# Kernel tuning notes

Measured on AMD Instinct MI355X. Metric: run time of the kernel, lower is better.

The kernel has to match this reference:

```python
import jax, jax.numpy as jnp
import numpy as np

B = 1_000_000
H = 64
TARGET = 0.62562059 * 10.0  # self.target * scale
# GRN constants from NETC_high.__init__
A1, A2, B1C, B2C, K, NEXP, S, SCALE = 1.0, 1.0, 0.2, 0.2, 1.1, 2, 0.5, 10.0


def setup_inputs() -> dict:
    key = jax.random.key(0)
    ks = jax.random.split(key, 10)
    def xavier(k, shape):
        fan_in, fan_out = shape[1], shape[0]
        std = (2.0 / (fan_in + fan_out)) ** 0.5
        return std * jax.random.normal(k, shape, dtype=jnp.float32)
    return {
        "x": jax.random.uniform(ks[0], (B,), dtype=jnp.float32) * 10.0,
        "y": jax.random.uniform(ks[1], (B,), dtype=jnp.float32) * 10.0,
        "e_x": 0.1 * jax.random.normal(ks[2], (B,), dtype=jnp.float32),
        "e_y": 0.1 * jax.random.normal(ks[3], (B,), dtype=jnp.float32),
        "W1": xavier(ks[4], (H, 2)),
        "b1": jnp.zeros((H,), dtype=jnp.float32),
        "W2": xavier(ks[5], (H, H)),
        "b2": jnp.zeros((H,), dtype=jnp.float32),
        "W3": xavier(ks[6], (1, H)),
        "b3": jnp.zeros((1,), dtype=jnp.float32),
    }


def _mlp(z, W1, b1, W2, b2, W3, b3):
    # ControlNet.function: Linear->ReLU->Linear->ReLU->Linear
    h = jax.nn.relu(z @ W1.T + b1)
    h = jax.nn.relu(h @ W2.T + b2)
    return h @ W3.T + b3  # [*, 1]


def _control(inp, W1, b1, W2, b2, W3, b3):
    # ControlNet.forward: u(x) - u(target)
    tgt = jnp.full((1, 2), TARGET, dtype=inp.dtype)
    return _mlp(inp, W1, b1, W2, b2, W3, b3) - _mlp(tgt, W1, b1, W2, b2, W3, b3)


def reference(x, y, e_x, e_y, W1, b1, W2, b2, W3, b3):
    inp = jnp.stack([x + e_x, y + e_y], axis=-1)  # [B, 2]
    u = _control(inp, W1, b1, W2, b2, W3, b3)[:, 0]  # [B]
    xs = x / SCALE
    ys = y / SCALE
    s2 = S ** NEXP
    hx = xs ** NEXP / (s2 + xs ** NEXP)   # Hill activation in x
    hy = ys ** NEXP / (s2 + ys ** NEXP)
    gx = s2 / (s2 + xs ** NEXP)           # Hill repression by x
    gy = s2 / (s2 + ys ** NEXP)
    dx = SCALE * (A1 * hx + B1C * gy - K * xs + u * hx)
    dy = SCALE * (A2 * hy + B2C * gx - K * ys)
    return (dx, dy, -dx, -dy)
```

## Files before the change

kernel.cpp:

```cpp
#include <hip/hip_runtime.h>

#define BTOT 1000000

typedef _Float16 f16;
typedef f16 f16x2 __attribute__((ext_vector_type(2)));
typedef f16 f16x8 __attribute__((ext_vector_type(8)));
typedef float f32x2 __attribute__((ext_vector_type(2)));
typedef float f32x4 __attribute__((ext_vector_type(4)));

#define WS_BFRAG 16
#define WS_W1A   8208
#define WS_W1B   10256
#define WS_B1P   12304
#define WS_W3V   14352
#define WS_B2V   15376

template<int CTRL>
__device__ __forceinline__ float dpp_add(float v) {
    int pv = __builtin_amdgcn_update_dpp(0, __builtin_bit_cast(int, v),
                                         CTRL, 0xF, 0xF, true);
    return v + __builtin_bit_cast(float, pv);
}
__device__ __forceinline__ float row_reduce16(float p) {
    p = dpp_add<0x128>(p);
    p = dpp_add<0x124>(p);
    p = dpp_add<0x122>(p);
    p = dpp_add<0x121>(p);
    return p;
}

__global__ __launch_bounds__(256) void setup_kernel(
    const float* __restrict__ W1, const float* __restrict__ b1,
    const float* __restrict__ W2, const float* __restrict__ b2,
    const float* __restrict__ W3, unsigned char* __restrict__ ws)
{
    const int tid  = threadIdx.x;
    const int quad = (tid & 63) >> 4;
    const int nl   = tid & 15;

    __shared__ float w2s[64 * 65];
    __shared__ float h1s[64];
    __shared__ float part[4 * 64];

    const float4* W2v = (const float4*)W2;
    #pragma unroll
    for (int r = 0; r < 4; ++r) {
        int idx = r * 256 + tid;
        float4 f = W2v[idx];
        int g = idx * 4, row = g >> 6, col = g & 63;
        float* p = &w2s[row * 65 + col];
        p[0] = f.x; p[1] = f.y; p[2] = f.z; p[3] = f.w;
    }
    const float T = 6.2562059f;
    if (tid < 64)
        h1s[tid] = fmaxf(0.f, W1[2 * tid] * T + W1[2 * tid + 1] * T + b1[tid]);
    __syncthreads();

    {
        int r = tid & 63, kq = tid >> 6;
        float p = 0.f;
        #pragma unroll
        for (int k = 0; k < 16; ++k)
            p = fmaf(w2s[r * 65 + kq * 16 + k], h1s[kq * 16 + k], p);
        part[kq * 64 + r] = p;
    }
    __syncthreads();
    if (tid < 64) {
        float h2 = b2[tid] + part[tid] + part[64 + tid] + part[128 + tid] + part[192 + tid];
        float pr = fmaxf(0.f, h2) * W3[tid];
        #pragma unroll
        for (int m = 1; m < 64; m <<= 1) pr += __shfl_xor(pr, m, 64);
        if (tid == 0) *(float*)ws = pr;
    }

    if (tid < 64) {
        f16x8* bfragT = (f16x8*)(ws + WS_BFRAG);
        #pragma unroll
        for (int n = 0; n < 4; ++n)
            #pragma unroll
            for (int ks = 0; ks < 2; ++ks) {
                f16x8 f;
                #pragma unroll
                for (int j = 0; j < 8; ++j)
                    f[j] = (f16)w2s[(n * 16 + nl) * 65 + ks * 32 + quad * 8 + j];
                bfragT[(n * 2 + ks) * 64 + tid] = f;
            }
        f16x2* w1aT = (f16x2*)(ws + WS_W1A);
        f16x2* w1bT = (f16x2*)(ws + WS_W1B);
        f16x2* b1pT = (f16x2*)(ws + WS_B1P);
        #pragma unroll
        for (int i = 0; i < 8; ++i) {
            int kk = (i < 4) ? (quad * 8 + 2 * i) : (32 + quad * 8 + 2 * (i - 4));
            w1aT[i * 64 + tid] = f16x2{(f16)W1[2 * kk],     (f16)W1[2 * kk + 2]};
            w1bT[i * 64 + tid] = f16x2{(f16)W1[2 * kk + 1], (f16)W1[2 * kk + 3]};
            b1pT[i * 64 + tid] = f16x2{(f16)b1[kk],         (f16)b1[kk + 1]};
        }
        float* w3vT = (float*)(ws + WS_W3V);
        float* b2vT = (float*)(ws + WS_B2V);
        #pragma unroll
        for (int n = 0; n < 4; ++n) {
            w3vT[n * 64 + tid] = W3[n * 16 + nl];
            b2vT[n * 64 + tid] = b2[n * 16 + nl];
        }
    }
}

__global__ __launch_bounds__(256, 4) void netc_kernel(
    const float* __restrict__ x,  const float* __restrict__ y,
    const float* __restrict__ ex, const float* __restrict__ ey,
    const unsigned char* __restrict__ ws,
    float* __restrict__ out)
{
    const int tid  = threadIdx.x;
    const int lane = tid & 63;
    const int wv   = tid >> 6;
    const int quad = lane >> 4;
    const int nl   = lane & 15;

    const float u_tgt = *(const float*)ws;
    const float one_minus_ut = 1.0f - u_tgt;
    const f16x8* bfragT = (const f16x8*)(ws + WS_BFRAG);
    f16x8 bfrag[4][2];
    #pragma unroll
    for (int n = 0; n < 4; ++n)
        #pragma unroll
        for (int ks = 0; ks < 2; ++ks)
            bfrag[n][ks] = bfragT[(n * 2 + ks) * 64 + lane];
    const f16x2* w1aT = (const f16x2*)(ws + WS_W1A);
    const f16x2* w1bT = (const f16x2*)(ws + WS_W1B);
    const f16x2* b1pT = (const f16x2*)(ws + WS_B1P);
    f16x2 w1a[8], w1b[8], b1p[8];
    #pragma unroll
    for (int i = 0; i < 8; ++i) {
        w1a[i] = w1aT[i * 64 + lane];
        w1b[i] = w1bT[i * 64 + lane];
        b1p[i] = b1pT[i * 64 + lane];
    }
    const float* w3vT = (const float*)(ws + WS_W3V);
    const float* b2vT = (const float*)(ws + WS_B2V);
    float w3v[4], b2v[4];
    #pragma unroll
    for (int n = 0; n < 4; ++n) { w3v[n] = w3vT[n * 64 + lane]; b2v[n] = b2vT[n * 64 + lane]; }

    const f16x2 zero2 = {(f16)0.f, (f16)0.f};
    const int nwaves = (gridDim.x * blockDim.x) >> 6;
    const int estep  = nwaves << 6;
    const int srcb = (((nl >> 2) << 4) + quad * 4 + (nl & 3)) << 2;

    int e0 = (((blockIdx.x << 2) + wv) << 6) + lane;

    float axv = 0.f, ayv = 0.f, aexv = 0.f, aeyv = 0.f;
    float bxv = 0.f, byv = 0.f, bexv = 0.f, beyv = 0.f;
    if (e0 < BTOT)         { axv = x[e0]; ayv = y[e0]; aexv = ex[e0]; aeyv = ey[e0]; }
    if (e0 + estep < BTOT) { int p = e0 + estep; bxv = x[p]; byv = y[p]; bexv = ex[p]; beyv = ey[p]; }

    auto body = [&](int ee, float& rx, float& ry, float& rex, float& rey) {
        float cx = rx, cy = ry, cex = rex, cey = rey;
        int pe = ee + 2 * estep;
        if (pe < BTOT) { rx = x[pe]; ry = y[pe]; rex = ex[pe]; rey = ey[pe]; }

        float av = cx + cex, bv = cy + cey;
        f16x2 pab = {(f16)av, (f16)bv};
        int pv = __builtin_bit_cast(int, pab);

        float xs = cx * 0.1f, ys = cy * 0.1f;
        float x2 = xs * xs, y2 = ys * ys;
        float invx = __fdividef(1.0f, 0.25f + x2);
        float invy = __fdividef(1.0f, 0.25f + y2);
        float hx = x2 * invx, hy = y2 * invy;
        float gx = 0.25f * invx, gy = 0.25f * invy;
        float cdx = 10.f * hx;
        float base_dx = fmaf(cdx, one_minus_ut, fmaf(2.f, gy, -11.f * xs));
        float dy = fmaf(10.f, hy, fmaf(2.f, gx, -11.f * ys));
        out[BTOT + ee]     = dy;
        out[3 * BTOT + ee] = -dy;

        f16x2 pt[4];
        #pragma unroll
        for (int t = 0; t < 4; ++t)
            pt[t] = __builtin_bit_cast(f16x2,
                __builtin_amdgcn_ds_bpermute((t * 16 + nl) << 2, pv));

        float ur[4];
        #pragma unroll
        for (int t = 0; t < 4; ++t) {
            f32x4 acc[4];
            #pragma unroll
            for (int n = 0; n < 4; ++n)
                acc[n] = f32x4{b2v[n], b2v[n], b2v[n], b2v[n]};

            f16x2 a2 = {pt[t][0], pt[t][0]};
            f16x2 bb = {pt[t][1], pt[t][1]};
            union { f16x2 h2[8]; f16x8 fr[2]; } u;
            #pragma unroll
            for (int i = 0; i < 8; ++i) {
                f16x2 h = a2 * w1a[i] + (bb * w1b[i] + b1p[i]);
                u.h2[i] = __builtin_elementwise_max(h, zero2);
            }
            #pragma unroll
            for (int n = 0; n < 4; ++n) {
                acc[n] = __builtin_amdgcn_mfma_f32_16x16x32_f16(u.fr[0], bfrag[n][0], acc[n], 0, 0, 0);
                acc[n] = __builtin_amdgcn_mfma_f32_16x16x32_f16(u.fr[1], bfrag[n][1], acc[n], 0, 0, 0);
            }

            f32x2 p01 = {0.f, 0.f}, p23 = {0.f, 0.f};
            #pragma unroll
            for (int n = 0; n < 4; ++n) {
                f32x2 lo = {acc[n][0], acc[n][1]};
                f32x2 hi = {acc[n][2], acc[n][3]};
                lo = __builtin_elementwise_max(lo, f32x2{0.f, 0.f});
                hi = __builtin_elementwise_max(hi, f32x2{0.f, 0.f});
                f32x2 w = {w3v[n], w3v[n]};
                p01 += lo * w;
                p23 += hi * w;
            }
            float u0 = row_reduce16(p01[0]);
            float u1 = row_reduce16(p01[1]);
            float u2 = row_reduce16(p23[0]);
            float u3 = row_reduce16(p23[1]);
            float v01 = (nl & 1) ? u1 : u0;
            float v23 = (nl & 1) ? u3 : u2;
            ur[t] = (nl & 2) ? v23 : v01;
        }

        float s01  = (nl & 4) ? ur[1] : ur[0];
        float s23  = (nl & 4) ? ur[3] : ur[2];
        float send = (nl & 8) ? s23 : s01;
        float u_raw = __builtin_bit_cast(float,
            __builtin_amdgcn_ds_bpermute(srcb, __builtin_bit_cast(int, send)));

        float dx = fmaf(cdx, u_raw, base_dx);
        out[ee]            = dx;
        out[2 * BTOT + ee] = -dx;
    };

    for (int e = e0; e < BTOT; e += 2 * estep) {
        body(e, axv, ayv, aexv, aeyv);
        int e1 = e + estep;
        if (e1 < BTOT)
            body(e1, bxv, byv, bexv, beyv);
    }
}

extern "C" void kernel_launch(void* const* d_in, const int* in_sizes, int n_in,
                              void* d_out, int out_size, void* d_ws, size_t ws_size,
                              hipStream_t stream) {
    const float* x  = (const float*)d_in[0];
    const float* y  = (const float*)d_in[1];
    const float* ex = (const float*)d_in[2];
    const float* ey = (const float*)d_in[3];
    const float* W1 = (const float*)d_in[4];
    const float* b1 = (const float*)d_in[5];
    const float* W2 = (const float*)d_in[6];
    const float* b2 = (const float*)d_in[7];
    const float* W3 = (const float*)d_in[8];
    float* out = (float*)d_out;
    unsigned char* ws = (unsigned char*)d_ws;

    setup_kernel<<<1, 256, 0, stream>>>(W1, b1, W2, b2, W3, ws);
    netc_kernel<<<1024, 256, 0, stream>>>(x, y, ex, ey, ws, out);
}
```

Before: 105.1 us.

## Fuse weight setup into main kernel, use DPP transpose-reduce, raise MFMA priority

Drops the separate single-block setup kernel. Each block now computes u(target) and builds its own fp16 MFMA fragments from W1/W2 in shared memory, which removes a launch and the serial dependency on the workspace. The four 16-lane row reductions per tile are replaced by a butterfly exchange (swap-and-add across xor-1/xor-2 lanes, then row shifts), which cuts the number of DPP ops. It also brackets the MFMA sequence with s_setprio. The trade-off is that every block redundantly recomputes the target MLP and adds about 17KB of shared memory, which may limit occupancy.

```diff
diff --git a/kernel.cpp b/kernel.cpp
--- a/kernel.cpp
+++ b/kernel.cpp
@@ -8,107 +8,27 @@
 typedef float f32x2 __attribute__((ext_vector_type(2)));
 typedef float f32x4 __attribute__((ext_vector_type(4)));
 
-#define WS_BFRAG 16
-#define WS_W1A   8208
-#define WS_W1B   10256
-#define WS_B1P   12304
-#define WS_W3V   14352
-#define WS_B2V   15376
-
 template<int CTRL>
 __device__ __forceinline__ float dpp_add(float v) {
     int pv = __builtin_amdgcn_update_dpp(0, __builtin_bit_cast(int, v),
                                          CTRL, 0xF, 0xF, true);
     return v + __builtin_bit_cast(float, pv);
 }
-__device__ __forceinline__ float row_reduce16(float p) {
-    p = dpp_add<0x128>(p);
-    p = dpp_add<0x124>(p);
-    p = dpp_add<0x122>(p);
-    p = dpp_add<0x121>(p);
-    return p;
-}
-
-__global__ __launch_bounds__(256) void setup_kernel(
-    const float* __restrict__ W1, const float* __restrict__ b1,
-    const float* __restrict__ W2, const float* __restrict__ b2,
-    const float* __restrict__ W3, unsigned char* __restrict__ ws)
-{
-    const int tid  = threadIdx.x;
-    const int quad = (tid & 63) >> 4;
-    const int nl   = tid & 15;
-
-    __shared__ float w2s[64 * 65];
-    __shared__ float h1s[64];
-    __shared__ float part[4 * 64];
-
-    const float4* W2v = (const float4*)W2;
-    #pragma unroll
-    for (int r = 0; r < 4; ++r) {
-        int idx = r * 256 + tid;
-        float4 f = W2v[idx];
-        int g = idx * 4, row = g >> 6, col = g & 63;
-        float* p = &w2s[row * 65 + col];
-        p[0] = f.x; p[1] = f.y; p[2] = f.z; p[3] = f.w;
-    }
-    const float T = 6.2562059f;
-    if (tid < 64)
-        h1s[tid] = fmaxf(0.f, W1[2 * tid] * T + W1[2 * tid + 1] * T + b1[tid]);
-    __syncthreads();
-
-    {
-        int r = tid & 63, kq = tid >> 6;
-        float p = 0.f;
-        #pragma unroll
-        for (int k = 0; k < 16; ++k)
-            p = fmaf(w2s[r * 65 + kq * 16 + k], h1s[kq * 16 + k], p);
-        part[kq * 64 + r] = p;
-    }
-    __syncthreads();
-    if (tid < 64) {
-        float h2 = b2[tid] + part[tid] + part[64 + tid] + part[128 + tid] + part[192 + tid];
-        float pr = fmaxf(0.f, h2) * W3[tid];
-        #pragma unroll
-        for (int m = 1; m < 64; m <<= 1) pr += __shfl_xor(pr, m, 64);
-        if (tid == 0) *(float*)ws = pr;
-    }
-
-    if (tid < 64) {
-        f16x8* bfragT = (f16x8*)(ws + WS_BFRAG);
-        #pragma unroll
-        for (int n = 0; n < 4; ++n)
-            #pragma unroll
-            for (int ks = 0; ks < 2; ++ks) {
-                f16x8 f;
-                #pragma unroll
-                for (int j = 0; j < 8; ++j)
-                    f[j] = (f16)w2s[(n * 16 + nl) * 65 + ks * 32 + quad * 8 + j];
-                bfragT[(n * 2 + ks) * 64 + tid] = f;
-            }
-        f16x2* w1aT = (f16x2*)(ws + WS_W1A);
-        f16x2* w1bT = (f16x2*)(ws + WS_W1B);
-        f16x2* b1pT = (f16x2*)(ws + WS_B1P);
-        #pragma unroll
-        for (int i = 0; i < 8; ++i) {
-            int kk = (i < 4) ? (quad * 8 + 2 * i) : (32 + quad * 8 + 2 * (i - 4));
-            w1aT[i * 64 + tid] = f16x2{(f16)W1[2 * kk],     (f16)W1[2 * kk + 2]};
-            w1bT[i * 64 + tid] = f16x2{(f16)W1[2 * kk + 1], (f16)W1[2 * kk + 3]};
-            b1pT[i * 64 + tid] = f16x2{(f16)b1[kk],         (f16)b1[kk + 1]};
-        }
-        float* w3vT = (float*)(ws + WS_W3V);
-        float* b2vT = (float*)(ws + WS_B2V);
-        #pragma unroll
-        for (int n = 0; n < 4; ++n) {
-            w3vT[n * 64 + tid] = W3[n * 16 + nl];
-            b2vT[n * 64 + tid] = b2[n * 16 + nl];
-        }
-    }
-}
+template<int CTRL>
+__device__ __forceinline__ float dpp_mov(float v) {
+    int pv = __builtin_amdgcn_update_dpp(0, __builtin_bit_cast(int, v),
+                                         CTRL, 0xF, 0xF, true);
+    return __builtin_bit_cast(float, pv);
+}
+#define DPP_XOR1 0xB1
+#define DPP_XOR2 0x4E
 
 __global__ __launch_bounds__(256, 4) void netc_kernel(
     const float* __restrict__ x,  const float* __restrict__ y,
     const float* __restrict__ ex, const float* __restrict__ ey,
-    const unsigned char* __restrict__ ws,
+    const float* __restrict__ W1, const float* __restrict__ b1,
+    const float* __restrict__ W2, const float* __restrict__ b2,
+    const float* __restrict__ W3,
     float* __restrict__ out)
 {
     const int tid  = threadIdx.x;
@@ -117,42 +37,81 @@
     const int quad = lane >> 4;
     const int nl   = lane & 15;
 
-    const float u_tgt = *(const float*)ws;
-    const float one_minus_ut = 1.0f - u_tgt;
-    const f16x8* bfragT = (const f16x8*)(ws + WS_BFRAG);
-    f16x8 bfrag[4][2];
-    #pragma unroll
-    for (int n = 0; n < 4; ++n)
-        #pragma unroll
-        for (int ks = 0; ks < 2; ++ks)
-            bfrag[n][ks] = bfragT[(n * 2 + ks) * 64 + lane];
-    const f16x2* w1aT = (const f16x2*)(ws + WS_W1A);
-    const f16x2* w1bT = (const f16x2*)(ws + WS_W1B);
-    const f16x2* b1pT = (const f16x2*)(ws + WS_B1P);
-    f16x2 w1a[8], w1b[8], b1p[8];
-    #pragma unroll
-    for (int i = 0; i < 8; ++i) {
-        w1a[i] = w1aT[i * 64 + lane];
-        w1b[i] = w1bT[i * 64 + lane];
-        b1p[i] = b1pT[i * 64 + lane];
-    }
-    const float* w3vT = (const float*)(ws + WS_W3V);
-    const float* b2vT = (const float*)(ws + WS_B2V);
-    float w3v[4], b2v[4];
-    #pragma unroll
-    for (int n = 0; n < 4; ++n) { w3v[n] = w3vT[n * 64 + lane]; b2v[n] = b2vT[n * 64 + lane]; }
-
-    const f16x2 zero2 = {(f16)0.f, (f16)0.f};
+    __shared__ float w2s[64 * 65];
+    __shared__ float h1s[64];
+    __shared__ float part[4 * 64];
+    __shared__ float utgt_s;
+
     const int nwaves = (gridDim.x * blockDim.x) >> 6;
     const int estep  = nwaves << 6;
-    const int srcb = (((nl >> 2) << 4) + quad * 4 + (nl & 3)) << 2;
-
     int e0 = (((blockIdx.x << 2) + wv) << 6) + lane;
 
     float axv = 0.f, ayv = 0.f, aexv = 0.f, aeyv = 0.f;
     float bxv = 0.f, byv = 0.f, bexv = 0.f, beyv = 0.f;
     if (e0 < BTOT)         { axv = x[e0]; ayv = y[e0]; aexv = ex[e0]; aeyv = ey[e0]; }
     if (e0 + estep < BTOT) { int p = e0 + estep; bxv = x[p]; byv = y[p]; bexv = ex[p]; beyv = ey[p]; }
+
+    {
+        const float4* W2v = (const float4*)W2;
+        #pragma unroll
+        for (int r = 0; r < 4; ++r) {
+            int idx = r * 256 + tid;
+            float4 f = W2v[idx];
+            int g = idx * 4, row = g >> 6, col = g & 63;
+            float* p = &w2s[row * 65 + col];
+            p[0] = f.x; p[1] = f.y; p[2] = f.z; p[3] = f.w;
+        }
+        const float T = 6.2562059f;
+        if (tid < 64)
+            h1s[tid] = fmaxf(0.f, W1[2 * tid] * T + W1[2 * tid + 1] * T + b1[tid]);
+        __syncthreads();
+        {
+            int r = tid & 63, kq = tid >> 6;
+            float p = 0.f;
+            #pragma unroll
+            for (int k = 0; k < 16; ++k)
+                p = fmaf(w2s[r * 65 + kq * 16 + k], h1s[kq * 16 + k], p);
+            part[kq * 64 + r] = p;
+        }
+        __syncthreads();
+        if (tid < 64) {
+            float h2 = b2[tid] + part[tid] + part[64 + tid] + part[128 + tid] + part[192 + tid];
+            float pr = fmaxf(0.f, h2) * W3[tid];
+            #pragma unroll
+            for (int m = 1; m < 64; m <<= 1) pr += __shfl_xor(pr, m, 64);
+            if (tid == 0) utgt_s = pr;
+        }
+        __syncthreads();
+    }
+    const float u_tgt = utgt_s;
+    const float one_minus_ut = 1.0f - u_tgt;
+
+    f16x8 bfrag[4][2];
+    #pragma unroll
+    for (int n = 0; n < 4; ++n)
+        #pragma unroll
+        for (int ks = 0; ks < 2; ++ks) {
+            f16x8 f;
+            #pragma unroll
+            for (int j = 0; j < 8; ++j)
+                f[j] = (f16)w2s[(n * 16 + nl) * 65 + ks * 32 + quad * 8 + j];
+            bfrag[n][ks] = f;
+        }
+    f16x2 w1a[8], w1b[8], b1p[8];
+    #pragma unroll
+    for (int i = 0; i < 8; ++i) {
+        int kk = (i < 4) ? (quad * 8 + 2 * i) : (32 + quad * 8 + 2 * (i - 4));
+        w1a[i] = f16x2{(f16)W1[2 * kk],     (f16)W1[2 * kk + 2]};
+        w1b[i] = f16x2{(f16)W1[2 * kk + 1], (f16)W1[2 * kk + 3]};
+        b1p[i] = f16x2{(f16)b1[kk],         (f16)b1[kk + 1]};
+    }
+    float w3v[4], b2v[4];
+    #pragma unroll
+    for (int n = 0; n < 4; ++n) { w3v[n] = W3[n * 16 + nl]; b2v[n] = b2[n * 16 + nl]; }
+
+    const f16x2 zero2 = {(f16)0.f, (f16)0.f};
+    const int srcb = (((nl >> 2) << 4) + quad * 4 + (nl & 3)) << 2;
+    const bool o1 = (nl & 1), o2 = (nl & 2);
 
     auto body = [&](int ee, float& rx, float& ry, float& rex, float& rey) {
         float cx = rx, cy = ry, cex = rex, cey = rey;
@@ -197,11 +156,13 @@
                 f16x2 h = a2 * w1a[i] + (bb * w1b[i] + b1p[i]);
                 u.h2[i] = __builtin_elementwise_max(h, zero2);
             }
+            __builtin_amdgcn_s_setprio(1);
             #pragma unroll
             for (int n = 0; n < 4; ++n) {
                 acc[n] = __builtin_amdgcn_mfma_f32_16x16x32_f16(u.fr[0], bfrag[n][0], acc[n], 0, 0, 0);
                 acc[n] = __builtin_amdgcn_mfma_f32_16x16x32_f16(u.fr[1], bfrag[n][1], acc[n], 0, 0, 0);
             }
+            __builtin_amdgcn_s_setprio(0);
 
             f32x2 p01 = {0.f, 0.f}, p23 = {0.f, 0.f};
             #pragma unroll
@@ -214,13 +175,18 @@
                 p01 += lo * w;
                 p23 += hi * w;
             }
-            float u0 = row_reduce16(p01[0]);
-            float u1 = row_reduce16(p01[1]);
-            float u2 = row_reduce16(p23[0]);
-            float u3 = row_reduce16(p23[1]);
-            float v01 = (nl & 1) ? u1 : u0;
-            float v23 = (nl & 1) ? u3 : u2;
-            ur[t] = (nl & 2) ? v23 : v01;
+            float a_keep = o1 ? p01[1] : p01[0];
+            float a_send = o1 ? p01[0] : p01[1];
+            float b_keep = o1 ? p23[1] : p23[0];
+            float b_send = o1 ? p23[0] : p23[1];
+            float a = a_keep + dpp_mov<DPP_XOR1>(a_send);
+            float b = b_keep + dpp_mov<DPP_XOR1>(b_send);
+            float c_keep = o2 ? b : a;
+            float c_send = o2 ? a : b;
+            float c = c_keep + dpp_mov<DPP_XOR2>(c_send);
+            c = dpp_add<0x124>(c);
+            c = dpp_add<0x128>(c);
+            ur[t] = c;
         }
 
         float s01  = (nl & 4) ? ur[1] : ur[0];
@@ -255,8 +221,7 @@
     const float* b2 = (const float*)d_in[7];
     const float* W3 = (const float*)d_in[8];
     float* out = (float*)d_out;
-    unsigned char* ws = (unsigned char*)d_ws;
-
-    setup_kernel<<<1, 256, 0, stream>>>(W1, b1, W2, b2, W3, ws);
-    netc_kernel<<<1024, 256, 0, stream>>>(x, y, ex, ey, ws, out);
-}
+    (void)d_ws; (void)ws_size;
+
+    netc_kernel<<<1024, 256, 0, stream>>>(x, y, ex, ey, W1, b1, W2, b2, W3, out);
+}
```

Measured after the change: 102.8 us. 1.02x faster.
